# Kernel optimization log

Hardware: AMD Instinct MI355X
Metric: run time of the kernel (lower is better)

The kernel has to match this reference:

```python
import jax, jax.numpy as jnp
import numpy as np

N = 50000
E = 500000
IN_DIM = 384
HID = 128
HEADS = 4
OUT_DIM = 384
NEG_SLOPE = 0.2


def gat_conv(x, edge_index, W, att_src, att_dst, bias):
    """PyG GATConv (concat=True, add_self_loops=True, eval mode).
    x: [N, F_in]; edge_index: [2, E] (row 0 = source j, row 1 = target i);
    W: [F_in, H*C]; att_src/att_dst: [H, C]; bias: [H*C].
    """
    n = x.shape[0]
    # add self loops
    loops = jnp.arange(n, dtype=edge_index.dtype)
    src = jnp.concatenate([edge_index[0], loops])
    dst = jnp.concatenate([edge_index[1], loops])

    h = (x @ W).reshape(n, HEADS, -1)              # [N, H, C]
    a_src = jnp.einsum('nhc,hc->nh', h, att_src)   # [N, H]
    a_dst = jnp.einsum('nhc,hc->nh', h, att_dst)   # [N, H]

    e = a_src[src] + a_dst[dst]                    # [E', H]
    e = jax.nn.leaky_relu(e, NEG_SLOPE)
    # segment softmax over incoming edges of each target node
    e_max = jax.ops.segment_max(e, dst, num_segments=n)
    e_exp = jnp.exp(e - e_max[dst])
    denom = jax.ops.segment_sum(e_exp, dst, num_segments=n)
    alpha = e_exp / denom[dst]                     # [E', H]

    msg = h[src] * alpha[:, :, None]               # [E', H, C]
    out = jax.ops.segment_sum(msg, dst, num_segments=n)  # [N, H, C]
    return out.reshape(n, -1) + bias


def setup_inputs() -> dict:
    key = jax.random.key(0)
    ks = jax.random.split(key, 12)
    s_in = 1.0 / np.sqrt(IN_DIM)
    s_h = 1.0 / np.sqrt(HEADS * HID)
    return {
        'x': jax.random.normal(ks[0], (N, IN_DIM), dtype=jnp.float32),
        'edge_index': jax.random.randint(ks[1], (2, E), 0, N, dtype=jnp.int32),
        'W1': jax.random.normal(ks[2], (IN_DIM, HEADS * HID), dtype=jnp.float32) * s_in,
        'a1_src': jax.random.normal(ks[3], (HEADS, HID), dtype=jnp.float32) * s_in,
        'a1_dst': jax.random.normal(ks[4], (HEADS, HID), dtype=jnp.float32) * s_in,
        'b1': jnp.zeros((HEADS * HID,), dtype=jnp.float32),
        'W2': jax.random.normal(ks[5], (HEADS * HID, HEADS * HID), dtype=jnp.float32) * s_h,
        'a2_src': jax.random.normal(ks[6], (HEADS, HID), dtype=jnp.float32) * s_h,
        'a2_dst': jax.random.normal(ks[7], (HEADS, HID), dtype=jnp.float32) * s_h,
        'b2': jnp.zeros((HEADS * HID,), dtype=jnp.float32),
        'Wfc': jax.random.normal(ks[8], (HEADS * HID, OUT_DIM), dtype=jnp.float32) * s_h,
        'bfc': jnp.zeros((OUT_DIM,), dtype=jnp.float32),
    }


def reference(x, edge_index, W1, a1_src, a1_dst, b1, W2, a2_src, a2_dst, b2, Wfc, bfc):
    h = jax.nn.relu(gat_conv(x, edge_index, W1, a1_src, a1_dst, b1))
    h = jax.nn.relu(gat_conv(h, edge_index, W2, a2_src, a2_dst, b2))
    return h @ Wfc + bfc  # [N, OUT_DIM]
```

## Files before the change

kernel.cpp:

```cpp
#include <hip/hip_runtime.h>
#include <cfloat>
#include <cstdint>

#define HEADS 4
#define HIDC 128
#define HC 512
#define NEG 0.2f

typedef _Float16 half8 __attribute__((ext_vector_type(8)));
typedef _Float16 half2v __attribute__((ext_vector_type(2)));
typedef float floatx4 __attribute__((ext_vector_type(4)));

__global__ __launch_bounds__(256) void mfma_gemm(
    const _Float16* __restrict__ A,
    const _Float16* __restrict__ Bt,
    _Float16* __restrict__ Ch,
    float* __restrict__ Cf,
    const float* __restrict__ bias,
    const float* __restrict__ atts,
    const float* __restrict__ attd,
    float* __restrict__ a_src,
    float* __restrict__ a_dst,
    int M, int N, int K)
{
    __shared__ __align__(16) _Float16 As[128 * 32];
    __shared__ __align__(16) _Float16 Bs[128 * 32];

    const int tid = threadIdx.x;
    const int w = tid >> 6;
    const int lane = tid & 63;
    const int wr = (w >> 1) * 64;
    const int wc = (w & 1) * 64;

    const int rowBase = blockIdx.y * 128;
    const int colBase = blockIdx.x * 128;

    const int sRow0 = (w * 2 + 0) * 16 + (lane >> 2);
    const int sRow1 = (w * 2 + 1) * 16 + (lane >> 2);
    const int sCol = (lane & 3) * 8;

    const _Float16* gA0 = A + (size_t)(rowBase + sRow0) * K + sCol;
    const _Float16* gA1 = A + (size_t)(rowBase + sRow1) * K + sCol;
    const _Float16* gB0 = Bt + (size_t)(colBase + sRow0) * K + sCol;
    const _Float16* gB1 = Bt + (size_t)(colBase + sRow1) * K + sCol;

    _Float16* lA0 = &As[(w * 2 + 0) * 512];
    _Float16* lA1 = &As[(w * 2 + 1) * 512];
    _Float16* lB0 = &Bs[(w * 2 + 0) * 512];
    _Float16* lB1 = &Bs[(w * 2 + 1) * 512];

    floatx4 acc[4][4];
#pragma unroll
    for (int i = 0; i < 4; i++)
#pragma unroll
        for (int j = 0; j < 4; j++) acc[i][j] = {0.f, 0.f, 0.f, 0.f};

    const int q = lane >> 4;
    const int l16 = lane & 15;

    for (int k0 = 0; k0 < K; k0 += 32) {
        __builtin_amdgcn_global_load_lds(
            (const __attribute__((address_space(1))) unsigned int*)(gA0 + k0),
            (__attribute__((address_space(3))) unsigned int*)lA0, 16, 0, 0);
        __builtin_amdgcn_global_load_lds(
            (const __attribute__((address_space(1))) unsigned int*)(gA1 + k0),
            (__attribute__((address_space(3))) unsigned int*)lA1, 16, 0, 0);
        __builtin_amdgcn_global_load_lds(
            (const __attribute__((address_space(1))) unsigned int*)(gB0 + k0),
            (__attribute__((address_space(3))) unsigned int*)lB0, 16, 0, 0);
        __builtin_amdgcn_global_load_lds(
            (const __attribute__((address_space(1))) unsigned int*)(gB1 + k0),
            (__attribute__((address_space(3))) unsigned int*)lB1, 16, 0, 0);
        __syncthreads();

        half8 af[4], bf[4];
#pragma unroll
        for (int i = 0; i < 4; i++)
            af[i] = *(const half8*)&As[(wr + i * 16 + l16) * 32 + q * 8];
#pragma unroll
        for (int j = 0; j < 4; j++)
            bf[j] = *(const half8*)&Bs[(wc + j * 16 + l16) * 32 + q * 8];
#pragma unroll
        for (int i = 0; i < 4; i++)
#pragma unroll
            for (int j = 0; j < 4; j++)
                acc[i][j] = __builtin_amdgcn_mfma_f32_16x16x32_f16(af[i], bf[j], acc[i][j], 0, 0, 0);
        __syncthreads();
    }

    if (Ch) {
#pragma unroll
        for (int i = 0; i < 4; i++)
#pragma unroll
            for (int j = 0; j < 4; j++) {
                const int col = colBase + wc + j * 16 + l16;
#pragma unroll
                for (int r = 0; r < 4; r++) {
                    const int row = rowBase + wr + i * 16 + q * 4 + r;
                    if (row < M) Ch[(size_t)row * N + col] = (_Float16)acc[i][j][r];
                }
            }
    }
    if (Cf) {
#pragma unroll
        for (int i = 0; i < 4; i++)
#pragma unroll
            for (int j = 0; j < 4; j++) {
                const int col = colBase + wc + j * 16 + l16;
                const float bb = bias ? bias[col] : 0.f;
#pragma unroll
                for (int r = 0; r < 4; r++) {
                    const int row = rowBase + wr + i * 16 + q * 4 + r;
                    if (row < M) Cf[(size_t)row * N + col] = acc[i][j][r] + bb;
                }
            }
    }

    if (atts) {
        float* ps = (float*)As;
        float* pd = ps + 256;
        const int head = blockIdx.x;
        float as[4], ad[4];
#pragma unroll
        for (int j = 0; j < 4; j++) {
            const int cl = wc + j * 16 + l16;
            as[j] = atts[head * HIDC + cl];
            ad[j] = attd[head * HIDC + cl];
        }
#pragma unroll
        for (int i = 0; i < 4; i++) {
#pragma unroll
            for (int r = 0; r < 4; r++) {
                float s_ = acc[i][0][r] * as[0] + acc[i][1][r] * as[1]
                         + acc[i][2][r] * as[2] + acc[i][3][r] * as[3];
                float d_ = acc[i][0][r] * ad[0] + acc[i][1][r] * ad[1]
                         + acc[i][2][r] * ad[2] + acc[i][3][r] * ad[3];
#pragma unroll
                for (int mk = 1; mk <= 8; mk <<= 1) {
                    s_ += __shfl_xor(s_, mk);
                    d_ += __shfl_xor(d_, mk);
                }
                if (l16 == 0) {
                    const int rloc = wr + i * 16 + q * 4 + r;
                    ps[(wc >> 6) * 128 + rloc] = s_;
                    pd[(wc >> 6) * 128 + rloc] = d_;
                }
            }
        }
        __syncthreads();
        if (tid < 128) {
            const int row = rowBase + tid;
            if (row < M) {
                a_src[(size_t)row * 4 + head] = ps[tid] + ps[128 + tid];
                a_dst[(size_t)row * 4 + head] = pd[tid] + pd[128 + tid];
            }
        }
    }
}

__global__ void convert_x_kernel(const float* __restrict__ x, _Float16* __restrict__ o, size_t nquads)
{
    size_t i = (size_t)blockIdx.x * blockDim.x + threadIdx.x;
    if (i < nquads) {
        float4 v = *(const float4*)(x + i * 4);
        _Float16* p = o + i * 4;
        p[0] = (_Float16)v.x; p[1] = (_Float16)v.y;
        p[2] = (_Float16)v.z; p[3] = (_Float16)v.w;
    }
}

__global__ void convert_wT_kernel(const float* __restrict__ W, _Float16* __restrict__ Wt, int K, int N)
{
    int k = blockIdx.x * 64 + (threadIdx.x & 63);
    int n = blockIdx.y * 4 + (threadIdx.x >> 6);
    if (k < K && n < N) Wt[(size_t)n * K + k] = (_Float16)W[(size_t)k * N + n];
}

__global__ void count_kernel(const int* __restrict__ dst, int* __restrict__ deg, int E)
{
    int e = blockIdx.x * blockDim.x + threadIdx.x;
    if (e < E) atomicAdd(&deg[dst[e]], 1);
}

__global__ __launch_bounds__(256) void block_sum_kernel(
    const int* __restrict__ deg, int* __restrict__ bsum, int Nn)
{
    int gid = blockIdx.x * 256 + threadIdx.x;
    int v = (gid < Nn) ? deg[gid] : 0;
#pragma unroll
    for (int o = 32; o >= 1; o >>= 1) v += __shfl_xor(v, o);
    __shared__ int ws[4];
    if ((threadIdx.x & 63) == 0) ws[threadIdx.x >> 6] = v;
    __syncthreads();
    if (threadIdx.x == 0) bsum[blockIdx.x] = ws[0] + ws[1] + ws[2] + ws[3];
}

__global__ __launch_bounds__(256) void scan_bsum_kernel(
    const int* __restrict__ bsum, int* __restrict__ bbase, int nb)
{
    __shared__ int s[256];
    const int tid = threadIdx.x;
    int v = (tid < nb) ? bsum[tid] : 0;
    s[tid] = v;
    __syncthreads();
    for (int off = 1; off < 256; off <<= 1) {
        int t = (tid >= off) ? s[tid - off] : 0;
        __syncthreads();
        s[tid] += t;
        __syncthreads();
    }
    if (tid < nb) bbase[tid] = s[tid] - v;
}

__global__ __launch_bounds__(256) void fill_rowptr_kernel(
    const int* __restrict__ deg, const int* __restrict__ bbase,
    int* __restrict__ rowptr, int* __restrict__ cursor, int Nn, int E)
{
    __shared__ int s[256];
    const int tid = threadIdx.x;
    const int gid = blockIdx.x * 256 + tid;
    int v = (gid < Nn) ? deg[gid] : 0;
    s[tid] = v;
    __syncthreads();
    for (int off = 1; off < 256; off <<= 1) {
        int t = (tid >= off) ? s[tid - off] : 0;
        __syncthreads();
        s[tid] += t;
        __syncthreads();
    }
    if (gid < Nn) {
        int r = bbase[blockIdx.x] + s[tid] - v;
        rowptr[gid] = r;
        cursor[gid] = r;
    }
    if (gid == 0) rowptr[Nn] = E;
}

__global__ void fill_kernel(const int* __restrict__ src, const int* __restrict__ dst,
                            int* __restrict__ cursor, int* __restrict__ eidx, int E)
{
    int e = blockIdx.x * blockDim.x + threadIdx.x;
    if (e < E) {
        int d = dst[e];
        int pos = atomicAdd(&cursor[d], 1);
        eidx[pos] = src[e];
    }
}

__global__ __launch_bounds__(256) void gather_kernel(
    const _Float16* __restrict__ h, const float* __restrict__ a_src,
    const float* __restrict__ a_dst,
    const int* __restrict__ rowptr, const int* __restrict__ eidx,
    const float* __restrict__ bias, _Float16* __restrict__ out, int Nn)
{
    const int wv = __builtin_amdgcn_readfirstlane(threadIdx.x >> 6);
    const int node = blockIdx.x * 4 + wv;
    if (node >= Nn) return;
    const int lane = threadIdx.x & 63;
    const int hd = lane >> 4;

    const int beg = rowptr[node];
    const int deg = rowptr[node + 1] - beg;

    const float ad = a_dst[(size_t)node * 4 + hd];
    const _Float16* hb = h + (size_t)lane * 8;

    float acc[8];
#pragma unroll
    for (int i = 0; i < 8; i++) acc[i] = 0.f;
    float dsum = 0.f;

    {
        const float as = a_src[(size_t)node * 4 + hd];
        half8 hv = *(const half8*)(hb + (size_t)node * HC);
        float l = as + ad; l = l > 0.f ? l : NEG * l;
        const float w = __expf(l);
        dsum += w;
#pragma unroll
        for (int i = 0; i < 8; i++) acc[i] += w * (float)hv[i];
    }

    int e = 0;
    for (; e + 2 <= deg; e += 2) {
        const int s0 = eidx[beg + e];
        const int s1 = eidx[beg + e + 1];
        half8 hv0 = *(const half8*)(hb + (size_t)s0 * HC);
        half8 hv1 = *(const half8*)(hb + (size_t)s1 * HC);
        const float as0 = a_src[(size_t)s0 * 4 + hd];
        const float as1 = a_src[(size_t)s1 * 4 + hd];
        float l0 = as0 + ad; l0 = l0 > 0.f ? l0 : NEG * l0;
        float l1 = as1 + ad; l1 = l1 > 0.f ? l1 : NEG * l1;
        const float w0 = __expf(l0);
        const float w1 = __expf(l1);
        dsum += w0 + w1;
#pragma unroll
        for (int i = 0; i < 8; i++) acc[i] += w0 * (float)hv0[i];
#pragma unroll
        for (int i = 0; i < 8; i++) acc[i] += w1 * (float)hv1[i];
    }
    if (e < deg) {
        const int s0 = eidx[beg + e];
        half8 hv0 = *(const half8*)(hb + (size_t)s0 * HC);
        const float as0 = a_src[(size_t)s0 * 4 + hd];
        float l0 = as0 + ad; l0 = l0 > 0.f ? l0 : NEG * l0;
        const float w0 = __expf(l0);
        dsum += w0;
#pragma unroll
        for (int i = 0; i < 8; i++) acc[i] += w0 * (float)hv0[i];
    }

    const float is = 1.f / dsum;
    const float* bp = bias + lane * 8;
    half8 ov;
#pragma unroll
    for (int i = 0; i < 8; i++) {
        float o = acc[i] * is + bp[i];
        o = o > 0.f ? o : 0.f;
        ov[i] = (_Float16)o;
    }
    *(half8*)(out + (size_t)node * HC + (size_t)lane * 8) = ov;
}

extern "C" void kernel_launch(void* const* d_in, const int* in_sizes, int n_in,
                              void* d_out, int out_size, void* d_ws, size_t ws_size,
                              hipStream_t stream)
{
    const float* x   = (const float*)d_in[0];
    const int*   ei  = (const int*)d_in[1];
    const float* W1  = (const float*)d_in[2];
    const float* a1s = (const float*)d_in[3];
    const float* a1d = (const float*)d_in[4];
    const float* b1  = (const float*)d_in[5];
    const float* W2  = (const float*)d_in[6];
    const float* a2s = (const float*)d_in[7];
    const float* a2d = (const float*)d_in[8];
    const float* b2  = (const float*)d_in[9];
    const float* Wfc = (const float*)d_in[10];
    const float* bfc = (const float*)d_in[11];
    float* out = (float*)d_out;

    const int Nn  = in_sizes[0] / 384;
    const int E   = in_sizes[1] / 2;
    const int IN  = 384;
    const int OUT = in_sizes[11];
    const int Mp  = ((Nn + 127) / 128) * 128;
    const int nb  = (Nn + 255) / 256;

    uint8_t* p = (uint8_t*)d_ws;
    auto alloc = [&](size_t bytes) {
        uint8_t* r = p;
        p += (bytes + 255) & ~(size_t)255;
        return r;
    };
    _Float16* Ah_x = (_Float16*)alloc((size_t)Mp * IN * 2);
    _Float16* Ah_g = (_Float16*)alloc((size_t)Mp * HC * 2);
    _Float16* Hh   = (_Float16*)alloc((size_t)Mp * HC * 2);
    _Float16* Wt1  = (_Float16*)alloc((size_t)HC * IN * 2);
    _Float16* Wt2  = (_Float16*)alloc((size_t)HC * HC * 2);
    _Float16* Wt3  = (_Float16*)alloc((size_t)OUT * HC * 2);
    float* a_src   = (float*)alloc((size_t)Nn * 4 * 4);
    float* a_dst   = (float*)alloc((size_t)Nn * 4 * 4);
    int* deg       = (int*)alloc((size_t)Nn * 4);
    int* rowptr    = (int*)alloc((size_t)(Nn + 1) * 4);
    int* cursor    = (int*)alloc((size_t)Nn * 4);
    int* eidx      = (int*)alloc((size_t)E * 4);
    int* bsum      = (int*)alloc((size_t)nb * 4);
    int* bbase     = (int*)alloc((size_t)nb * 4);

    const int* e_src = ei;
    const int* e_dst = ei + E;

    {
        size_t nq = (size_t)Nn * IN / 4;
        convert_x_kernel<<<(nq + 255) / 256, 256, 0, stream>>>(x, Ah_x, nq);
        dim3 gw1((IN + 63) / 64, HC / 4);
        convert_wT_kernel<<<gw1, 256, 0, stream>>>(W1, Wt1, IN, HC);
        dim3 gw2((HC + 63) / 64, HC / 4);
        convert_wT_kernel<<<gw2, 256, 0, stream>>>(W2, Wt2, HC, HC);
        dim3 gw3((HC + 63) / 64, OUT / 4);
        convert_wT_kernel<<<gw3, 256, 0, stream>>>(Wfc, Wt3, HC, OUT);
    }

    hipMemsetAsync(deg, 0, Nn * sizeof(int), stream);
    const int eb = (E + 255) / 256;
    count_kernel<<<eb, 256, 0, stream>>>(e_dst, deg, E);
    block_sum_kernel<<<nb, 256, 0, stream>>>(deg, bsum, Nn);
    scan_bsum_kernel<<<1, 256, 0, stream>>>(bsum, bbase, nb);
    fill_rowptr_kernel<<<nb, 256, 0, stream>>>(deg, bbase, rowptr, cursor, Nn, E);
    fill_kernel<<<eb, 256, 0, stream>>>(e_src, e_dst, cursor, eidx, E);

    const dim3 gg1(HC / 128, Mp / 128);
    const int gb = (Nn + 3) / 4;

    mfma_gemm<<<gg1, 256, 0, stream>>>(Ah_x, Wt1, Hh, nullptr, nullptr,
                                       a1s, a1d, a_src, a_dst, Nn, HC, IN);
    gather_kernel<<<gb, 256, 0, stream>>>(Hh, a_src, a_dst, rowptr, eidx, b1, Ah_g, Nn);

    mfma_gemm<<<gg1, 256, 0, stream>>>(Ah_g, Wt2, Hh, nullptr, nullptr,
                                       a2s, a2d, a_src, a_dst, Nn, HC, HC);
    gather_kernel<<<gb, 256, 0, stream>>>(Hh, a_src, a_dst, rowptr, eidx, b2, Ah_g, Nn);

    const dim3 gg3(OUT / 128, Mp / 128);
    mfma_gemm<<<gg3, 256, 0, stream>>>(Ah_g, Wt3, nullptr, out, bfc,
                                       nullptr, nullptr, nullptr, nullptr, Nn, OUT, HC);
}
```

Baseline: 564.5 us.

## Batch edge index loads via wave shuffles and add XCD-aware GEMM block remap

```diff
diff --git a/kernel.cpp b/kernel.cpp
--- a/kernel.cpp
+++ b/kernel.cpp
@@ -8,7 +8,6 @@
 #define NEG 0.2f
 
 typedef _Float16 half8 __attribute__((ext_vector_type(8)));
-typedef _Float16 half2v __attribute__((ext_vector_type(2)));
 typedef float floatx4 __attribute__((ext_vector_type(4)));
 
 __global__ __launch_bounds__(256) void mfma_gemm(
@@ -26,14 +25,24 @@
     __shared__ __align__(16) _Float16 As[128 * 32];
     __shared__ __align__(16) _Float16 Bs[128 * 32];
 
+    const int nwg = gridDim.x * gridDim.y;
+    int lin = blockIdx.y * gridDim.x + blockIdx.x;
+    {
+        const int q = nwg >> 3, r = nwg & 7;
+        const int xcd = lin & 7, pos = lin >> 3;
+        lin = (xcd < r ? xcd * (q + 1) : r * (q + 1) + (xcd - r) * q) + pos;
+    }
+    const int bx = lin % gridDim.x;
+    const int by = lin / gridDim.x;
+
     const int tid = threadIdx.x;
     const int w = tid >> 6;
     const int lane = tid & 63;
     const int wr = (w >> 1) * 64;
     const int wc = (w & 1) * 64;
 
-    const int rowBase = blockIdx.y * 128;
-    const int colBase = blockIdx.x * 128;
+    const int rowBase = by * 128;
+    const int colBase = bx * 128;
 
     const int sRow0 = (w * 2 + 0) * 16 + (lane >> 2);
     const int sRow1 = (w * 2 + 1) * 16 + (lane >> 2);
@@ -55,7 +64,7 @@
 #pragma unroll
         for (int j = 0; j < 4; j++) acc[i][j] = {0.f, 0.f, 0.f, 0.f};
 
-    const int q = lane >> 4;
+    const int q16 = lane >> 4;
     const int l16 = lane & 15;
 
     for (int k0 = 0; k0 < K; k0 += 32) {
@@ -76,10 +85,10 @@
         half8 af[4], bf[4];
 #pragma unroll
         for (int i = 0; i < 4; i++)
-            af[i] = *(const half8*)&As[(wr + i * 16 + l16) * 32 + q * 8];
+            af[i] = *(const half8*)&As[(wr + i * 16 + l16) * 32 + q16 * 8];
 #pragma unroll
         for (int j = 0; j < 4; j++)
-            bf[j] = *(const half8*)&Bs[(wc + j * 16 + l16) * 32 + q * 8];
+            bf[j] = *(const half8*)&Bs[(wc + j * 16 + l16) * 32 + q16 * 8];
 #pragma unroll
         for (int i = 0; i < 4; i++)
 #pragma unroll
@@ -96,7 +105,7 @@
                 const int col = colBase + wc + j * 16 + l16;
 #pragma unroll
                 for (int r = 0; r < 4; r++) {
-                    const int row = rowBase + wr + i * 16 + q * 4 + r;
+                    const int row = rowBase + wr + i * 16 + q16 * 4 + r;
                     if (row < M) Ch[(size_t)row * N + col] = (_Float16)acc[i][j][r];
                 }
             }
@@ -110,7 +119,7 @@
                 const float bb = bias ? bias[col] : 0.f;
 #pragma unroll
                 for (int r = 0; r < 4; r++) {
-                    const int row = rowBase + wr + i * 16 + q * 4 + r;
+                    const int row = rowBase + wr + i * 16 + q16 * 4 + r;
                     if (row < M) Cf[(size_t)row * N + col] = acc[i][j][r] + bb;
                 }
             }
@@ -119,7 +128,7 @@
     if (atts) {
         float* ps = (float*)As;
         float* pd = ps + 256;
-        const int head = blockIdx.x;
+        const int head = bx;
         float as[4], ad[4];
 #pragma unroll
         for (int j = 0; j < 4; j++) {
@@ -141,7 +150,7 @@
                     d_ += __shfl_xor(d_, mk);
                 }
                 if (l16 == 0) {
-                    const int rloc = wr + i * 16 + q * 4 + r;
+                    const int rloc = wr + i * 16 + q16 * 4 + r;
                     ps[(wc >> 6) * 128 + rloc] = s_;
                     pd[(wc >> 6) * 128 + rloc] = d_;
                 }
@@ -261,6 +270,7 @@
 
     const int beg = rowptr[node];
     const int deg = rowptr[node + 1] - beg;
+    const int total = deg + 1;
 
     const float ad = a_dst[(size_t)node * 4 + hd];
     const _Float16* hb = h + (size_t)lane * 8;
@@ -270,43 +280,39 @@
     for (int i = 0; i < 8; i++) acc[i] = 0.f;
     float dsum = 0.f;
 
-    {
-        const float as = a_src[(size_t)node * 4 + hd];
-        half8 hv = *(const half8*)(hb + (size_t)node * HC);
-        float l = as + ad; l = l > 0.f ? l : NEG * l;
-        const float w = __expf(l);
-        dsum += w;
-#pragma unroll
-        for (int i = 0; i < 8; i++) acc[i] += w * (float)hv[i];
-    }
-
-    int e = 0;
-    for (; e + 2 <= deg; e += 2) {
-        const int s0 = eidx[beg + e];
-        const int s1 = eidx[beg + e + 1];
-        half8 hv0 = *(const half8*)(hb + (size_t)s0 * HC);
-        half8 hv1 = *(const half8*)(hb + (size_t)s1 * HC);
-        const float as0 = a_src[(size_t)s0 * 4 + hd];
-        const float as1 = a_src[(size_t)s1 * 4 + hd];
-        float l0 = as0 + ad; l0 = l0 > 0.f ? l0 : NEG * l0;
-        float l1 = as1 + ad; l1 = l1 > 0.f ? l1 : NEG * l1;
-        const float w0 = __expf(l0);
-        const float w1 = __expf(l1);
-        dsum += w0 + w1;
-#pragma unroll
-        for (int i = 0; i < 8; i++) acc[i] += w0 * (float)hv0[i];
-#pragma unroll
-        for (int i = 0; i < 8; i++) acc[i] += w1 * (float)hv1[i];
-    }
-    if (e < deg) {
-        const int s0 = eidx[beg + e];
-        half8 hv0 = *(const half8*)(hb + (size_t)s0 * HC);
-        const float as0 = a_src[(size_t)s0 * 4 + hd];
-        float l0 = as0 + ad; l0 = l0 > 0.f ? l0 : NEG * l0;
-        const float w0 = __expf(l0);
-        dsum += w0;
-#pragma unroll
-        for (int i = 0; i < 8; i++) acc[i] += w0 * (float)hv0[i];
+    for (int base = 0; base < total; base += 64) {
+        const int cnt = min(total - base, 64);
+        const int t = base + lane;
+        int myIdx = node;
+        if (t < deg) myIdx = eidx[beg + t];
+
+        for (int e = 0; e < cnt; e += 4) {
+            const int s0 = __shfl(myIdx, e);
+            const int s1 = __shfl(myIdx, e + 1);
+            const int s2 = __shfl(myIdx, e + 2);
+            const int s3 = __shfl(myIdx, e + 3);
+            half8 hv0 = *(const half8*)(hb + (size_t)s0 * HC);
+            half8 hv1 = *(const half8*)(hb + (size_t)s1 * HC);
+            half8 hv2 = *(const half8*)(hb + (size_t)s2 * HC);
+            half8 hv3 = *(const half8*)(hb + (size_t)s3 * HC);
+            const float as0 = a_src[(size_t)s0 * 4 + hd];
+            const float as1 = a_src[(size_t)s1 * 4 + hd];
+            const float as2 = a_src[(size_t)s2 * 4 + hd];
+            const float as3 = a_src[(size_t)s3 * 4 + hd];
+            float l0 = as0 + ad; l0 = l0 > 0.f ? l0 : NEG * l0;
+            float l1 = as1 + ad; l1 = l1 > 0.f ? l1 : NEG * l1;
+            float l2 = as2 + ad; l2 = l2 > 0.f ? l2 : NEG * l2;
+            float l3 = as3 + ad; l3 = l3 > 0.f ? l3 : NEG * l3;
+            const float w0 = __expf(l0);
+            const float w1 = (e + 1 < cnt) ? __expf(l1) : 0.f;
+            const float w2 = (e + 2 < cnt) ? __expf(l2) : 0.f;
+            const float w3 = (e + 3 < cnt) ? __expf(l3) : 0.f;
+            dsum += (w0 + w1) + (w2 + w3);
+#pragma unroll
+            for (int i = 0; i < 8; i++)
+                acc[i] += (w0 * (float)hv0[i] + w1 * (float)hv1[i])
+                        + (w2 * (float)hv2[i] + w3 * (float)hv3[i]);
+        }
     }
 
     const float is = 1.f / dsum;
```

Measured after the change: 549.3 us. -2.7%, faster.
